# Performance work log

Hardware: AMD Instinct MI355X
Metric: run time of the kernel (lower is better)

The kernel has to match this reference:

```python
import jax, jax.numpy as jnp
import numpy as np
import math

B, S, D, H = 2, 2048, 1024, 16
DK = D // H


def setup_inputs() -> dict:
    key = jax.random.key(0)
    ks = jax.random.split(key, 11)
    f = jnp.float32
    return {
        "query": jax.random.normal(ks[0], (B, S, D), f),
        "key": jax.random.normal(ks[1], (B, S, D), f),
        "value": jax.random.normal(ks[2], (B, S, D), f),
        "wq": jax.random.normal(ks[3], (D, D), f) * 0.02,
        "bq": jnp.zeros((D,), f),
        "wk": jax.random.normal(ks[4], (D, D), f) * 0.02,
        "bk": jnp.zeros((D,), f),
        "wv": jax.random.normal(ks[5], (D, D), f) * 0.02,
        "bv": jnp.zeros((D,), f),
        "wo": jax.random.normal(ks[6], (D, D), f) * 0.02,
        "bo": jnp.zeros((D,), f),
    }


def reference(query, key, value, wq, bq, wk, bk, wv, bv, wo, bo):
    # Linear projections (torch Linear: y = x @ W.T + b)
    q = query @ wq.T + bq
    k = key @ wk.T + bk
    v = value @ wv.T + bv
    # [B,S,D] -> [B,H,S,DK]
    q = q.reshape(B, S, H, DK).transpose(0, 2, 1, 3)
    k = k.reshape(B, S, H, DK).transpose(0, 2, 1, 3)
    v = v.reshape(B, S, H, DK).transpose(0, 2, 1, 3)
    scores = jnp.einsum("bhqd,bhkd->bhqk", q, k) / math.sqrt(DK)
    causal = jnp.triu(jnp.ones((S, S), dtype=bool), k=1)  # strict upper triangle masked
    scores = jnp.where(causal, -jnp.inf, scores)
    attn = jax.nn.softmax(scores, axis=-1)  # dropout is identity in eval (p=0)
    x = jnp.einsum("bhqk,bhkd->bhqd", attn, v)
    x = x.transpose(0, 2, 1, 3).reshape(B, S, D)
    return x @ wo.T + bo
```

## Files before the change

kernel.cpp:

```cpp
#include <hip/hip_runtime.h>
#include <math.h>

#define BB 2
#define SS 2048
#define DD 1024
#define HH 16
#define DKK 64
#define MM (BB * SS)
#define KK DD
#define VSTR 2176

typedef __attribute__((ext_vector_type(8))) short short8;
typedef __attribute__((ext_vector_type(4))) float floatx4;

__device__ inline unsigned short f2bf(float x) {
    unsigned int u = __float_as_uint(x);
    u += 0x7fffu + ((u >> 16) & 1u);
    return (unsigned short)(u >> 16);
}

__device__ inline void cast4f(const float* __restrict__ in, unsigned short* __restrict__ out, int i) {
    const float4 v = *(const float4*)(in + i);
    unsigned long long pk = (unsigned long long)f2bf(v.x)
                          | ((unsigned long long)f2bf(v.y) << 16)
                          | ((unsigned long long)f2bf(v.z) << 32)
                          | ((unsigned long long)f2bf(v.w) << 48);
    *(unsigned long long*)(out + i) = pk;
}

__global__ __launch_bounds__(256) void cast3(const float* __restrict__ a, const float* __restrict__ b,
                                             const float* __restrict__ c,
                                             unsigned short* __restrict__ oa, unsigned short* __restrict__ ob,
                                             unsigned short* __restrict__ oc) {
    const int w = blockIdx.y;
    const float* in = (w == 0) ? a : (w == 1) ? b : c;
    unsigned short* out = (w == 0) ? oa : (w == 1) ? ob : oc;
    cast4f(in, out, (blockIdx.x * 256 + threadIdx.x) * 4);
}

__global__ __launch_bounds__(256) void cast4w(const float* __restrict__ a, const float* __restrict__ b,
                                              const float* __restrict__ c, const float* __restrict__ d,
                                              unsigned short* __restrict__ oa, unsigned short* __restrict__ ob,
                                              unsigned short* __restrict__ oc, unsigned short* __restrict__ od) {
    const int w = blockIdx.y;
    const float* in = (w == 0) ? a : (w == 1) ? b : (w == 2) ? c : d;
    unsigned short* out = (w == 0) ? oa : (w == 1) ? ob : (w == 2) ? oc : od;
    cast4f(in, out, (blockIdx.x * 256 + threadIdx.x) * 4);
}

#define GLDS(gp, lp) __builtin_amdgcn_global_load_lds( \
    (const __attribute__((address_space(1))) void*)(gp), \
    (__attribute__((address_space(3))) void*)(lp), 16, 0, 0)

__device__ __forceinline__ void gemm_body(const unsigned short* __restrict__ A,
                                          const unsigned short* __restrict__ W,
                                          const float* __restrict__ bias,
                                          void* __restrict__ Cout, int mode, int blk,
                                          unsigned short* As, unsigned short* Bs) {
    const int t    = threadIdx.x;
    const int lane = t & 63;
    const int wave = t >> 6;
    const int col  = lane & 15;
    const int quad = lane >> 4;

    const int m0  = (blk & 63) * 64;
    const int n0  = (blk >> 6) * 128;
    const int wm0 = (wave & 1) * 32;
    const int wn0 = (wave >> 1) * 64;

    const int sw = ((t & 3) ^ ((t >> 3) & 3)) * 8;
    const size_t arow = (size_t)(m0 + (t >> 2)) * KK + sw;
    const size_t brow = (size_t)(n0 + (t >> 2)) * KK + sw;
    const int rseg = (quad ^ ((col >> 1) & 3)) * 8;

    floatx4 acc[2][4] = {};

    GLDS(A + arow,           &As[(t >> 2) * 32 + sw]);
    GLDS(W + brow,           &Bs[(t >> 2) * 32 + sw]);
    GLDS(W + brow + 64 * KK, &Bs[(64 + (t >> 2)) * 32 + sw]);

    int cur = 0;
    for (int kb = 0; kb < KK / 32; ++kb) {
        __syncthreads();

        if (kb + 1 < KK / 32) {
            const int k0 = (kb + 1) * 32;
            const int nx = cur ^ 1;
            GLDS(A + arow + k0,           &As[nx * 64 * 32 + (t >> 2) * 32 + sw]);
            GLDS(W + brow + k0,           &Bs[nx * 128 * 32 + (t >> 2) * 32 + sw]);
            GLDS(W + brow + k0 + 64 * KK, &Bs[nx * 128 * 32 + (64 + (t >> 2)) * 32 + sw]);
        }

        const unsigned short* Ab = &As[cur * 64 * 32];
        const unsigned short* Bb = &Bs[cur * 128 * 32];
        short8 a[2], b[4];
        #pragma unroll
        for (int i = 0; i < 2; ++i)
            a[i] = *(const short8*)(Ab + (wm0 + i * 16 + col) * 32 + rseg);
        #pragma unroll
        for (int j = 0; j < 4; ++j)
            b[j] = *(const short8*)(Bb + (wn0 + j * 16 + col) * 32 + rseg);

        #pragma unroll
        for (int i = 0; i < 2; ++i)
            #pragma unroll
            for (int j = 0; j < 4; ++j)
                acc[i][j] = __builtin_amdgcn_mfma_f32_16x16x32_bf16(a[i], b[j], acc[i][j], 0, 0, 0);

        cur ^= 1;
    }

    #pragma unroll
    for (int i = 0; i < 2; ++i) {
        #pragma unroll
        for (int j = 0; j < 4; ++j) {
            const int n  = n0 + wn0 + j * 16 + col;
            const float bv = bias[n];
            const int h = n / DKK, dk = n % DKK;
            #pragma unroll
            for (int r = 0; r < 4; ++r) {
                const int m = m0 + wm0 + i * 16 + quad * 4 + r;
                const int bdx = m / SS, s = m % SS;
                const float v = acc[i][j][r] + bv;
                if (mode == 0) {
                    ((unsigned short*)Cout)[(((size_t)(bdx * HH + h)) * SS + s) * DKK + dk] = f2bf(v);
                } else if (mode == 1) {
                    ((unsigned short*)Cout)[(((size_t)(bdx * HH + h)) * DKK + dk) * VSTR + s] = f2bf(v);
                } else {
                    ((float*)Cout)[(size_t)m * DD + n] = v;
                }
            }
        }
    }
}

__global__ __launch_bounds__(256) void gemm_qkv(const unsigned short* __restrict__ qB,
                                                const unsigned short* __restrict__ kB,
                                                const unsigned short* __restrict__ vB,
                                                const unsigned short* __restrict__ wqB,
                                                const unsigned short* __restrict__ wkB,
                                                const unsigned short* __restrict__ wvB,
                                                const float* __restrict__ bq,
                                                const float* __restrict__ bk,
                                                const float* __restrict__ bv,
                                                unsigned short* __restrict__ Qh,
                                                unsigned short* __restrict__ Kh,
                                                unsigned short* __restrict__ Vt) {
    __shared__ __align__(16) unsigned short As[2 * 64 * 32];
    __shared__ __align__(16) unsigned short Bs[2 * 128 * 32];
    const int which = blockIdx.x >> 9;
    const int blk   = blockIdx.x & 511;
    if (which == 0)      gemm_body(qB, wqB, bq, Qh, 0, blk, As, Bs);
    else if (which == 1) gemm_body(kB, wkB, bk, Kh, 0, blk, As, Bs);
    else                 gemm_body(vB, wvB, bv, Vt, 1, blk, As, Bs);
}

__global__ __launch_bounds__(256) void gemm_out(const unsigned short* __restrict__ A,
                                                const unsigned short* __restrict__ W,
                                                const float* __restrict__ bias,
                                                float* __restrict__ C) {
    __shared__ __align__(16) unsigned short As[2 * 64 * 32];
    __shared__ __align__(16) unsigned short Bs[2 * 128 * 32];
    gemm_body(A, W, bias, C, 2, blockIdx.x, As, Bs);
}

#define C1 0.18033688011112042f
#define C2 11.541560327111707f

#define MFMA __builtin_amdgcn_mfma_f32_16x16x32_bf16

#define SOFTPV(j0v, vv)                                                                              \
    {                                                                                                \
        if ((j0v) + 31 > q0) {                                                                       \
            _Pragma("unroll")                                                                        \
            for (int r = 0; r < 4; ++r) {                                                            \
                const int row = q0 + quad * 4 + r;                                                   \
                const float p0 = ((j0v) + col      <= row) ? __builtin_exp2f(fmaf(sc0[r], C1, -C2)) : 0.f; \
                const float p1 = ((j0v) + 16 + col <= row) ? __builtin_exp2f(fmaf(sc1[r], C1, -C2)) : 0.f; \
                lp[r] += p0 + p1;                                                                    \
                Pw[(quad * 4 + r) * 40 + col]      = (unsigned short)(__float_as_uint(p0) >> 16);    \
                Pw[(quad * 4 + r) * 40 + col + 16] = (unsigned short)(__float_as_uint(p1) >> 16);    \
            }                                                                                        \
        } else {                                                                                     \
            _Pragma("unroll")                                                                        \
            for (int r = 0; r < 4; ++r) {                                                            \
                const float p0 = __builtin_exp2f(fmaf(sc0[r], C1, -C2));                             \
                const float p1 = __builtin_exp2f(fmaf(sc1[r], C1, -C2));                             \
                lp[r] += p0 + p1;                                                                    \
                Pw[(quad * 4 + r) * 40 + col]      = (unsigned short)(__float_as_uint(p0) >> 16);    \
                Pw[(quad * 4 + r) * 40 + col + 16] = (unsigned short)(__float_as_uint(p1) >> 16);    \
            }                                                                                        \
        }                                                                                            \
        const short8 pa = *(const short8*)(Pw + col * 40 + quad * 8);                                \
        o0 = MFMA(pa, vv##0, o0, 0, 0, 0);                                                           \
        o1 = MFMA(pa, vv##1, o1, 0, 0, 0);                                                           \
        o2 = MFMA(pa, vv##2, o2, 0, 0, 0);                                                           \
        o3 = MFMA(pa, vv##3, o3, 0, 0, 0);                                                           \
    }

__global__ __launch_bounds__(256) void attn_mfma(const unsigned short* __restrict__ Qh,
                                                 const unsigned short* __restrict__ Kh,
                                                 const unsigned short* __restrict__ Vt,
                                                 unsigned short* __restrict__ X) {
    __shared__ __align__(16) unsigned short Ks[2][32 * 64];
    __shared__ __align__(16) unsigned short Vs[2][64 * 32];
    __shared__ unsigned short Plds[4][16 * 40];

    const int t    = threadIdx.x;
    const int lane = t & 63;
    const int wave = t >> 6;
    const int col  = lane & 15;
    const int quad = lane >> 4;

    const int lin = blockIdx.x;
    const int bh  = (lin & 7) + 8 * ((lin >> 3) & 3);
    const int c   = 31 - (lin >> 5);
    const int b   = bh / HH, h = bh % HH;

    const unsigned short* Kb = Kh + (size_t)bh * SS * DKK;
    const unsigned short* Vb = Vt + (size_t)bh * DKK * VSTR;

    const int kRow = t >> 3;
    const int kSeg = ((t & 7) ^ (kRow & 7)) * 8;
    const int vRow = t >> 2;
    const int vSeg = (t & 3) * 8;

    const int q0 = c * 64 + wave * 16;
    unsigned short* Pw = &Plds[wave][0];

    const unsigned short* Qb = Qh + ((size_t)bh * SS + q0) * DKK;
    const short8 qa0 = *(const short8*)(Qb + (size_t)col * DKK + quad * 8);
    const short8 qa1 = *(const short8*)(Qb + (size_t)col * DKK + 32 + quad * 8);

    floatx4 o0 = {0.f, 0.f, 0.f, 0.f}, o1 = o0, o2 = o0, o3 = o0;
    float lp[4] = {0.f, 0.f, 0.f, 0.f};

    const int nkb = 2 * (c + 1);

    const int ks0 = ((quad     ^ (col & 7)) << 3);
    const int ks1 = (((quad|4) ^ (col & 7)) << 3);

    GLDS(Kb + (size_t)kRow * DKK + kSeg, &Ks[0][t * 8]);
    GLDS(Vb + (size_t)vRow * VSTR + vSeg, &Vs[0][t * 8]);

    int cur = 0;
    for (int kb = 0; kb < nkb; ++kb) {
        __syncthreads();

        if (kb + 1 < nkb) {
            const int jn = (kb + 1) * 32;
            const int nx = cur ^ 1;
            GLDS(Kb + (size_t)(jn + kRow) * DKK + kSeg, &Ks[nx][t * 8]);
            GLDS(Vb + (size_t)vRow * VSTR + jn + vSeg, &Vs[nx][t * 8]);
        }

        const int j0 = kb * 32;
        if (j0 < q0 + 16) {
            const unsigned short* Kp = &Ks[cur][0];
            const short8 k0 = *(const short8*)(Kp + col * 64 + ks0);
            const short8 k1 = *(const short8*)(Kp + col * 64 + ks1);
            const short8 k2 = *(const short8*)(Kp + (col + 16) * 64 + ks0);
            const short8 k3 = *(const short8*)(Kp + (col + 16) * 64 + ks1);

            floatx4 sc0 = {0.f, 0.f, 0.f, 0.f}, sc1 = sc0;
            sc0 = MFMA(qa0, k0, sc0, 0, 0, 0);
            sc0 = MFMA(qa1, k1, sc0, 0, 0, 0);
            sc1 = MFMA(qa0, k2, sc1, 0, 0, 0);
            sc1 = MFMA(qa1, k3, sc1, 0, 0, 0);

            const unsigned short* Vp = &Vs[cur][0];
            short8 vv0 = *(const short8*)(Vp + (col)      * 32 + quad * 8);
            short8 vv1 = *(const short8*)(Vp + (col + 16) * 32 + quad * 8);
            short8 vv2 = *(const short8*)(Vp + (col + 32) * 32 + quad * 8);
            short8 vv3 = *(const short8*)(Vp + (col + 48) * 32 + quad * 8);

            SOFTPV(j0, vv)
        }

        cur ^= 1;
    }

    #pragma unroll
    for (int r = 0; r < 4; ++r) {
        float s = lp[r];
        s += __shfl_xor(s, 1, 64);
        s += __shfl_xor(s, 2, 64);
        s += __shfl_xor(s, 4, 64);
        s += __shfl_xor(s, 8, 64);
        lp[r] = 1.f / s;
    }

    unsigned short* Xp = X + ((size_t)(b * SS + q0 + quad * 4)) * DD + h * DKK + col;
    #pragma unroll
    for (int r = 0; r < 4; ++r) {
        Xp[(size_t)r * DD + 0]  = f2bf(o0[r] * lp[r]);
        Xp[(size_t)r * DD + 16] = f2bf(o1[r] * lp[r]);
        Xp[(size_t)r * DD + 32] = f2bf(o2[r] * lp[r]);
        Xp[(size_t)r * DD + 48] = f2bf(o3[r] * lp[r]);
    }
}

extern "C" void kernel_launch(void* const* d_in, const int* in_sizes, int n_in,
                              void* d_out, int out_size, void* d_ws, size_t ws_size,
                              hipStream_t stream) {
    const float* query = (const float*)d_in[0];
    const float* key   = (const float*)d_in[1];
    const float* value = (const float*)d_in[2];
    const float* wq    = (const float*)d_in[3];
    const float* bq    = (const float*)d_in[4];
    const float* wk    = (const float*)d_in[5];
    const float* bk    = (const float*)d_in[6];
    const float* wv    = (const float*)d_in[7];
    const float* bv    = (const float*)d_in[8];
    const float* wo    = (const float*)d_in[9];
    const float* bo    = (const float*)d_in[10];

    char* ws = (char*)d_ws;
    const size_t MB = 1024 * 1024;
    unsigned short* qB  = (unsigned short*)(ws);
    unsigned short* kB  = (unsigned short*)(ws + 8 * MB);
    unsigned short* vB  = (unsigned short*)(ws + 16 * MB);
    unsigned short* wqB = (unsigned short*)(ws + 24 * MB);
    unsigned short* wkB = (unsigned short*)(ws + 26 * MB);
    unsigned short* wvB = (unsigned short*)(ws + 28 * MB);
    unsigned short* woB = (unsigned short*)(ws + 30 * MB);
    unsigned short* Qh  = (unsigned short*)(ws + 32 * MB);
    unsigned short* Kh  = (unsigned short*)(ws + 40 * MB);
    unsigned short* Vt  = (unsigned short*)(ws + 48 * MB);
    unsigned short* Xb  = qB;

    cast3<<<dim3(4096, 3), 256, 0, stream>>>(query, key, value, qB, kB, vB);
    cast4w<<<dim3(1024, 4), 256, 0, stream>>>(wq, wk, wv, wo, wqB, wkB, wvB, woB);

    gemm_qkv<<<1536, 256, 0, stream>>>(qB, kB, vB, wqB, wkB, wvB, bq, bk, bv, Qh, Kh, Vt);

    attn_mfma<<<1024, 256, 0, stream>>>(Qh, Kh, Vt, Xb);

    gemm_out<<<512, 256, 0, stream>>>(Xb, woB, bo, (float*)d_out);
}
```

Baseline: 250.3 us.

## Merge cast kernels, enlarge QKV GEMM tiles, restructure attention with 64-key stages

The two cast kernels become one launch. The QKV projection GEMM now uses its own kernel with 128x128 tiles (4x4 MFMA per wave) in place of the shared 64x128 body, halving the block count. Attention now stages 64 keys per iteration and computes the transposed product (K·Q, V·P), so each lane owns a query row: the row sum needs fewer shuffles, P goes to LDS as packed words, and outputs are written as vectorized uint2. The trade-off is more LDS and registers, which can lower occupancy.

```diff
diff --git a/kernel.cpp b/kernel.cpp
--- a/kernel.cpp
+++ b/kernel.cpp
@@ -19,6 +19,10 @@
     return (unsigned short)(u >> 16);
 }
 
+__device__ inline unsigned int pkbf(float a, float b) {
+    return (__float_as_uint(b) & 0xffff0000u) | (__float_as_uint(a) >> 16);
+}
+
 __device__ inline void cast4f(const float* __restrict__ in, unsigned short* __restrict__ out, int i) {
     const float4 v = *(const float4*)(in + i);
     unsigned long long pk = (unsigned long long)f2bf(v.x)
@@ -28,24 +32,30 @@
     *(unsigned long long*)(out + i) = pk;
 }
 
-__global__ __launch_bounds__(256) void cast3(const float* __restrict__ a, const float* __restrict__ b,
-                                             const float* __restrict__ c,
-                                             unsigned short* __restrict__ oa, unsigned short* __restrict__ ob,
-                                             unsigned short* __restrict__ oc) {
-    const int w = blockIdx.y;
-    const float* in = (w == 0) ? a : (w == 1) ? b : c;
-    unsigned short* out = (w == 0) ? oa : (w == 1) ? ob : oc;
-    cast4f(in, out, (blockIdx.x * 256 + threadIdx.x) * 4);
-}
-
-__global__ __launch_bounds__(256) void cast4w(const float* __restrict__ a, const float* __restrict__ b,
-                                              const float* __restrict__ c, const float* __restrict__ d,
-                                              unsigned short* __restrict__ oa, unsigned short* __restrict__ ob,
-                                              unsigned short* __restrict__ oc, unsigned short* __restrict__ od) {
-    const int w = blockIdx.y;
-    const float* in = (w == 0) ? a : (w == 1) ? b : (w == 2) ? c : d;
-    unsigned short* out = (w == 0) ? oa : (w == 1) ? ob : (w == 2) ? oc : od;
-    cast4f(in, out, (blockIdx.x * 256 + threadIdx.x) * 4);
+__global__ __launch_bounds__(256) void cast_all(const float* __restrict__ q, const float* __restrict__ k,
+                                                const float* __restrict__ v,
+                                                const float* __restrict__ wq, const float* __restrict__ wk,
+                                                const float* __restrict__ wv, const float* __restrict__ wo,
+                                                unsigned short* __restrict__ oq, unsigned short* __restrict__ ok,
+                                                unsigned short* __restrict__ ov,
+                                                unsigned short* __restrict__ owq, unsigned short* __restrict__ owk,
+                                                unsigned short* __restrict__ owv, unsigned short* __restrict__ owo) {
+    const int blk = blockIdx.x;
+    const float* in;
+    unsigned short* out;
+    int idx;
+    if (blk < 12288) {
+        const int w = blk >> 12;
+        idx = blk & 4095;
+        in  = (w == 0) ? q : (w == 1) ? k : v;
+        out = (w == 0) ? oq : (w == 1) ? ok : ov;
+    } else {
+        const int w = (blk - 12288) >> 10;
+        idx = (blk - 12288) & 1023;
+        in  = (w == 0) ? wq : (w == 1) ? wk : (w == 2) ? wv : wo;
+        out = (w == 0) ? owq : (w == 1) ? owk : (w == 2) ? owv : owo;
+    }
+    cast4f(in, out, (idx * 256 + threadIdx.x) * 4);
 }
 
 #define GLDS(gp, lp) __builtin_amdgcn_global_load_lds( \
@@ -116,22 +126,15 @@
         for (int j = 0; j < 4; ++j) {
             const int n  = n0 + wn0 + j * 16 + col;
             const float bv = bias[n];
-            const int h = n / DKK, dk = n % DKK;
             #pragma unroll
             for (int r = 0; r < 4; ++r) {
                 const int m = m0 + wm0 + i * 16 + quad * 4 + r;
-                const int bdx = m / SS, s = m % SS;
                 const float v = acc[i][j][r] + bv;
-                if (mode == 0) {
-                    ((unsigned short*)Cout)[(((size_t)(bdx * HH + h)) * SS + s) * DKK + dk] = f2bf(v);
-                } else if (mode == 1) {
-                    ((unsigned short*)Cout)[(((size_t)(bdx * HH + h)) * DKK + dk) * VSTR + s] = f2bf(v);
-                } else {
-                    ((float*)Cout)[(size_t)m * DD + n] = v;
-                }
+                ((float*)Cout)[(size_t)m * DD + n] = v;
             }
         }
     }
+    (void)mode;
 }
 
 __global__ __launch_bounds__(256) void gemm_qkv(const unsigned short* __restrict__ qB,
@@ -146,13 +149,91 @@
                                                 unsigned short* __restrict__ Qh,
                                                 unsigned short* __restrict__ Kh,
                                                 unsigned short* __restrict__ Vt) {
-    __shared__ __align__(16) unsigned short As[2 * 64 * 32];
+    __shared__ __align__(16) unsigned short As[2 * 128 * 32];
     __shared__ __align__(16) unsigned short Bs[2 * 128 * 32];
-    const int which = blockIdx.x >> 9;
-    const int blk   = blockIdx.x & 511;
-    if (which == 0)      gemm_body(qB, wqB, bq, Qh, 0, blk, As, Bs);
-    else if (which == 1) gemm_body(kB, wkB, bk, Kh, 0, blk, As, Bs);
-    else                 gemm_body(vB, wvB, bv, Vt, 1, blk, As, Bs);
+
+    const int which = blockIdx.x >> 8;
+    const int blk   = blockIdx.x & 255;
+    const unsigned short* A = (which == 0) ? qB : (which == 1) ? kB : vB;
+    const unsigned short* W = (which == 0) ? wqB : (which == 1) ? wkB : wvB;
+    const float* bias       = (which == 0) ? bq : (which == 1) ? bk : bv;
+
+    const int t    = threadIdx.x;
+    const int lane = t & 63;
+    const int wave = t >> 6;
+    const int col  = lane & 15;
+    const int quad = lane >> 4;
+
+    const int m0  = (blk & 31) * 128;
+    const int n0  = (blk >> 5) * 128;
+    const int wm0 = (wave & 1) * 64;
+    const int wn0 = (wave >> 1) * 64;
+
+    const int sw = ((t & 3) ^ ((t >> 3) & 3)) * 8;
+    const size_t arow = (size_t)(m0 + (t >> 2)) * KK + sw;
+    const size_t brow = (size_t)(n0 + (t >> 2)) * KK + sw;
+    const int rseg = (quad ^ ((col >> 1) & 3)) * 8;
+
+    floatx4 acc[4][4] = {};
+
+    GLDS(A + arow,           &As[(t >> 2) * 32 + sw]);
+    GLDS(A + arow + 64 * KK, &As[(64 + (t >> 2)) * 32 + sw]);
+    GLDS(W + brow,           &Bs[(t >> 2) * 32 + sw]);
+    GLDS(W + brow + 64 * KK, &Bs[(64 + (t >> 2)) * 32 + sw]);
+
+    int cur = 0;
+    for (int kb = 0; kb < KK / 32; ++kb) {
+        __syncthreads();
+
+        if (kb + 1 < KK / 32) {
+            const int k0 = (kb + 1) * 32;
+            const int nx = cur ^ 1;
+            GLDS(A + arow + k0,           &As[nx * 128 * 32 + (t >> 2) * 32 + sw]);
+            GLDS(A + arow + k0 + 64 * KK, &As[nx * 128 * 32 + (64 + (t >> 2)) * 32 + sw]);
+            GLDS(W + brow + k0,           &Bs[nx * 128 * 32 + (t >> 2) * 32 + sw]);
+            GLDS(W + brow + k0 + 64 * KK, &Bs[nx * 128 * 32 + (64 + (t >> 2)) * 32 + sw]);
+        }
+
+        const unsigned short* Ab = &As[cur * 128 * 32];
+        const unsigned short* Bb = &Bs[cur * 128 * 32];
+        short8 a[4], b[4];
+        #pragma unroll
+        for (int i = 0; i < 4; ++i)
+            a[i] = *(const short8*)(Ab + (wm0 + i * 16 + col) * 32 + rseg);
+        #pragma unroll
+        for (int j = 0; j < 4; ++j)
+            b[j] = *(const short8*)(Bb + (wn0 + j * 16 + col) * 32 + rseg);
+
+        #pragma unroll
+        for (int i = 0; i < 4; ++i)
+            #pragma unroll
+            for (int j = 0; j < 4; ++j)
+                acc[i][j] = __builtin_amdgcn_mfma_f32_16x16x32_bf16(a[i], b[j], acc[i][j], 0, 0, 0);
+
+        cur ^= 1;
+    }
+
+    #pragma unroll
+    for (int i = 0; i < 4; ++i) {
+        #pragma unroll
+        for (int j = 0; j < 4; ++j) {
+            const int n  = n0 + wn0 + j * 16 + col;
+            const float bv = bias[n];
+            const int h = n / DKK, dk = n % DKK;
+            #pragma unroll
+            for (int r = 0; r < 4; ++r) {
+                const int m = m0 + wm0 + i * 16 + quad * 4 + r;
+                const int bdx = m / SS, s = m % SS;
+                const float v = acc[i][j][r] + bv;
+                if (which != 2) {
+                    unsigned short* O = (which == 0) ? Qh : Kh;
+                    O[(((size_t)(bdx * HH + h)) * SS + s) * DKK + dk] = f2bf(v);
+                } else {
+                    Vt[(((size_t)(bdx * HH + h)) * DKK + dk) * VSTR + s] = f2bf(v);
+                }
+            }
+        }
+    }
 }
 
 __global__ __launch_bounds__(256) void gemm_out(const unsigned short* __restrict__ A,
@@ -166,45 +247,15 @@
 
 #define C1 0.18033688011112042f
 #define C2 11.541560327111707f
-
 #define MFMA __builtin_amdgcn_mfma_f32_16x16x32_bf16
-
-#define SOFTPV(j0v, vv)                                                                              \
-    {                                                                                                \
-        if ((j0v) + 31 > q0) {                                                                       \
-            _Pragma("unroll")                                                                        \
-            for (int r = 0; r < 4; ++r) {                                                            \
-                const int row = q0 + quad * 4 + r;                                                   \
-                const float p0 = ((j0v) + col      <= row) ? __builtin_exp2f(fmaf(sc0[r], C1, -C2)) : 0.f; \
-                const float p1 = ((j0v) + 16 + col <= row) ? __builtin_exp2f(fmaf(sc1[r], C1, -C2)) : 0.f; \
-                lp[r] += p0 + p1;                                                                    \
-                Pw[(quad * 4 + r) * 40 + col]      = (unsigned short)(__float_as_uint(p0) >> 16);    \
-                Pw[(quad * 4 + r) * 40 + col + 16] = (unsigned short)(__float_as_uint(p1) >> 16);    \
-            }                                                                                        \
-        } else {                                                                                     \
-            _Pragma("unroll")                                                                        \
-            for (int r = 0; r < 4; ++r) {                                                            \
-                const float p0 = __builtin_exp2f(fmaf(sc0[r], C1, -C2));                             \
-                const float p1 = __builtin_exp2f(fmaf(sc1[r], C1, -C2));                             \
-                lp[r] += p0 + p1;                                                                    \
-                Pw[(quad * 4 + r) * 40 + col]      = (unsigned short)(__float_as_uint(p0) >> 16);    \
-                Pw[(quad * 4 + r) * 40 + col + 16] = (unsigned short)(__float_as_uint(p1) >> 16);    \
-            }                                                                                        \
-        }                                                                                            \
-        const short8 pa = *(const short8*)(Pw + col * 40 + quad * 8);                                \
-        o0 = MFMA(pa, vv##0, o0, 0, 0, 0);                                                           \
-        o1 = MFMA(pa, vv##1, o1, 0, 0, 0);                                                           \
-        o2 = MFMA(pa, vv##2, o2, 0, 0, 0);                                                           \
-        o3 = MFMA(pa, vv##3, o3, 0, 0, 0);                                                           \
-    }
 
 __global__ __launch_bounds__(256) void attn_mfma(const unsigned short* __restrict__ Qh,
                                                  const unsigned short* __restrict__ Kh,
                                                  const unsigned short* __restrict__ Vt,
                                                  unsigned short* __restrict__ X) {
-    __shared__ __align__(16) unsigned short Ks[2][32 * 64];
-    __shared__ __align__(16) unsigned short Vs[2][64 * 32];
-    __shared__ unsigned short Plds[4][16 * 40];
+    __shared__ __align__(16) unsigned short Ks[2][64 * 64];
+    __shared__ __align__(16) unsigned short Vs[2][64 * 64];
+    __shared__ __align__(16) unsigned short Plds[4][16 * 40];
 
     const int t    = threadIdx.x;
     const int lane = t & 63;
@@ -220,10 +271,10 @@
     const unsigned short* Kb = Kh + (size_t)bh * SS * DKK;
     const unsigned short* Vb = Vt + (size_t)bh * DKK * VSTR;
 
-    const int kRow = t >> 3;
-    const int kSeg = ((t & 7) ^ (kRow & 7)) * 8;
-    const int vRow = t >> 2;
-    const int vSeg = (t & 3) * 8;
+    const int r0  = t >> 3;
+    const int r1  = (t + 256) >> 3;
+    const int sg0 = ((t & 7) ^ (r0 & 7)) * 8;
+    const int sg1 = ((t & 7) ^ (r1 & 7)) * 8;
 
     const int q0 = c * 64 + wave * 16;
     unsigned short* Pw = &Plds[wave][0];
@@ -233,70 +284,106 @@
     const short8 qa1 = *(const short8*)(Qb + (size_t)col * DKK + 32 + quad * 8);
 
     floatx4 o0 = {0.f, 0.f, 0.f, 0.f}, o1 = o0, o2 = o0, o3 = o0;
-    float lp[4] = {0.f, 0.f, 0.f, 0.f};
-
-    const int nkb = 2 * (c + 1);
-
-    const int ks0 = ((quad     ^ (col & 7)) << 3);
-    const int ks1 = (((quad|4) ^ (col & 7)) << 3);
-
-    GLDS(Kb + (size_t)kRow * DKK + kSeg, &Ks[0][t * 8]);
-    GLDS(Vb + (size_t)vRow * VSTR + vSeg, &Vs[0][t * 8]);
+    float lp = 0.f;
+
+    const int nst = c + 1;
+
+    const int ksA = ((quad)      ^ (col & 7)) * 8;
+    const int ksB = ((quad | 4)  ^ (col & 7)) * 8;
+
+    GLDS(Kb + (size_t)r0 * DKK + sg0,  &Ks[0][t * 8]);
+    GLDS(Kb + (size_t)r1 * DKK + sg1,  &Ks[0][(t + 256) * 8]);
+    GLDS(Vb + (size_t)r0 * VSTR + sg0, &Vs[0][t * 8]);
+    GLDS(Vb + (size_t)r1 * VSTR + sg1, &Vs[0][(t + 256) * 8]);
 
     int cur = 0;
-    for (int kb = 0; kb < nkb; ++kb) {
+    for (int kb = 0; kb < nst; ++kb) {
         __syncthreads();
 
-        if (kb + 1 < nkb) {
-            const int jn = (kb + 1) * 32;
+        if (kb + 1 < nst) {
+            const int jn = (kb + 1) * 64;
             const int nx = cur ^ 1;
-            GLDS(Kb + (size_t)(jn + kRow) * DKK + kSeg, &Ks[nx][t * 8]);
-            GLDS(Vb + (size_t)vRow * VSTR + jn + vSeg, &Vs[nx][t * 8]);
-        }
-
-        const int j0 = kb * 32;
-        if (j0 < q0 + 16) {
-            const unsigned short* Kp = &Ks[cur][0];
-            const short8 k0 = *(const short8*)(Kp + col * 64 + ks0);
-            const short8 k1 = *(const short8*)(Kp + col * 64 + ks1);
-            const short8 k2 = *(const short8*)(Kp + (col + 16) * 64 + ks0);
-            const short8 k3 = *(const short8*)(Kp + (col + 16) * 64 + ks1);
-
-            floatx4 sc0 = {0.f, 0.f, 0.f, 0.f}, sc1 = sc0;
-            sc0 = MFMA(qa0, k0, sc0, 0, 0, 0);
-            sc0 = MFMA(qa1, k1, sc0, 0, 0, 0);
-            sc1 = MFMA(qa0, k2, sc1, 0, 0, 0);
-            sc1 = MFMA(qa1, k3, sc1, 0, 0, 0);
-
-            const unsigned short* Vp = &Vs[cur][0];
-            short8 vv0 = *(const short8*)(Vp + (col)      * 32 + quad * 8);
-            short8 vv1 = *(const short8*)(Vp + (col + 16) * 32 + quad * 8);
-            short8 vv2 = *(const short8*)(Vp + (col + 32) * 32 + quad * 8);
-            short8 vv3 = *(const short8*)(Vp + (col + 48) * 32 + quad * 8);
-
-            SOFTPV(j0, vv)
+            GLDS(Kb + (size_t)(jn + r0) * DKK + sg0,  &Ks[nx][t * 8]);
+            GLDS(Kb + (size_t)(jn + r1) * DKK + sg1,  &Ks[nx][(t + 256) * 8]);
+            GLDS(Vb + (size_t)r0 * VSTR + jn + sg0,   &Vs[nx][t * 8]);
+            GLDS(Vb + (size_t)r1 * VSTR + jn + sg1,   &Vs[nx][(t + 256) * 8]);
+        }
+
+        const unsigned short* Kp = &Ks[cur][0];
+        const unsigned short* Vp = &Vs[cur][0];
+
+        #pragma unroll
+        for (int hh = 0; hh < 2; ++hh) {
+            const int j0 = kb * 64 + hh * 32;
+            if (j0 < q0 + 16) {
+                const short8 k0 = *(const short8*)(Kp + (hh * 32 + col) * 64 + ksA);
+                const short8 k1 = *(const short8*)(Kp + (hh * 32 + col) * 64 + ksB);
+                const short8 k2 = *(const short8*)(Kp + (hh * 32 + col + 16) * 64 + ksA);
+                const short8 k3 = *(const short8*)(Kp + (hh * 32 + col + 16) * 64 + ksB);
+
+                floatx4 t0 = {0.f, 0.f, 0.f, 0.f}, t1 = t0;
+                t0 = MFMA(k0, qa0, t0, 0, 0, 0);
+                t0 = MFMA(k1, qa1, t0, 0, 0, 0);
+                t1 = MFMA(k2, qa0, t1, 0, 0, 0);
+                t1 = MFMA(k3, qa1, t1, 0, 0, 0);
+
+                float p[8];
+                if (j0 + 31 > q0) {
+                    const int lim = q0 + col - j0;
+                    #pragma unroll
+                    for (int r = 0; r < 4; ++r) {
+                        p[r]     = (quad * 4 + r      <= lim) ? __builtin_exp2f(fmaf(t0[r], C1, -C2)) : 0.f;
+                        p[4 + r] = (16 + quad * 4 + r <= lim) ? __builtin_exp2f(fmaf(t1[r], C1, -C2)) : 0.f;
+                    }
+                } else {
+                    #pragma unroll
+                    for (int r = 0; r < 4; ++r) {
+                        p[r]     = __builtin_exp2f(fmaf(t0[r], C1, -C2));
+                        p[4 + r] = __builtin_exp2f(fmaf(t1[r], C1, -C2));
+                    }
+                }
+                lp += (p[0] + p[1]) + (p[2] + p[3]) + (p[4] + p[5]) + (p[6] + p[7]);
+
+                uint2 w0 = { pkbf(p[0], p[1]), pkbf(p[2], p[3]) };
+                uint2 w1 = { pkbf(p[4], p[5]), pkbf(p[6], p[7]) };
+                *(uint2*)(Pw + col * 40 + quad * 4)      = w0;
+                *(uint2*)(Pw + col * 40 + 16 + quad * 4) = w1;
+
+                const short8 pb = *(const short8*)(Pw + col * 40 + quad * 8);
+                const int vs = hh ? ksB : ksA;
+                const short8 v0 = *(const short8*)(Vp + (col)      * 64 + vs);
+                const short8 v1 = *(const short8*)(Vp + (col + 16) * 64 + vs);
+                const short8 v2 = *(const short8*)(Vp + (col + 32) * 64 + vs);
+                const short8 v3 = *(const short8*)(Vp + (col + 48) * 64 + vs);
+                o0 = MFMA(v0, pb, o0, 0, 0, 0);
+                o1 = MFMA(v1, pb, o1, 0, 0, 0);
+                o2 = MFMA(v2, pb, o2, 0, 0, 0);
+                o3 = MFMA(v3, pb, o3, 0, 0, 0);
+            }
         }
 
         cur ^= 1;
     }
 
-    #pragma unroll
-    for (int r = 0; r < 4; ++r) {
-        float s = lp[r];
-        s += __shfl_xor(s, 1, 64);
-        s += __shfl_xor(s, 2, 64);
-        s += __shfl_xor(s, 4, 64);
-        s += __shfl_xor(s, 8, 64);
-        lp[r] = 1.f / s;
-    }
-
-    unsigned short* Xp = X + ((size_t)(b * SS + q0 + quad * 4)) * DD + h * DKK + col;
-    #pragma unroll
-    for (int r = 0; r < 4; ++r) {
-        Xp[(size_t)r * DD + 0]  = f2bf(o0[r] * lp[r]);
-        Xp[(size_t)r * DD + 16] = f2bf(o1[r] * lp[r]);
-        Xp[(size_t)r * DD + 32] = f2bf(o2[r] * lp[r]);
-        Xp[(size_t)r * DD + 48] = f2bf(o3[r] * lp[r]);
+    lp += __shfl_xor(lp, 16, 64);
+    lp += __shfl_xor(lp, 32, 64);
+    const float li = 1.f / lp;
+
+    unsigned short* Xp = X + ((size_t)(b * SS + q0 + col)) * DD + h * DKK + quad * 4;
+    {
+        uint2 w;
+        w.x = (unsigned int)f2bf(o0[0] * li) | ((unsigned int)f2bf(o0[1] * li) << 16);
+        w.y = (unsigned int)f2bf(o0[2] * li) | ((unsigned int)f2bf(o0[3] * li) << 16);
+        *(uint2*)(Xp + 0) = w;
+        w.x = (unsigned int)f2bf(o1[0] * li) | ((unsigned int)f2bf(o1[1] * li) << 16);
+        w.y = (unsigned int)f2bf(o1[2] * li) | ((unsigned int)f2bf(o1[3] * li) << 16);
+        *(uint2*)(Xp + 16) = w;
+        w.x = (unsigned int)f2bf(o2[0] * li) | ((unsigned int)f2bf(o2[1] * li) << 16);
+        w.y = (unsigned int)f2bf(o2[2] * li) | ((unsigned int)f2bf(o2[3] * li) << 16);
+        *(uint2*)(Xp + 32) = w;
+        w.x = (unsigned int)f2bf(o3[0] * li) | ((unsigned int)f2bf(o3[1] * li) << 16);
+        w.y = (unsigned int)f2bf(o3[2] * li) | ((unsigned int)f2bf(o3[3] * li) << 16);
+        *(uint2*)(Xp + 48) = w;
     }
 }
 
@@ -329,10 +416,10 @@
     unsigned short* Vt  = (unsigned short*)(ws + 48 * MB);
     unsigned short* Xb  = qB;
 
-    cast3<<<dim3(4096, 3), 256, 0, stream>>>(query, key, value, qB, kB, vB);
-    cast4w<<<dim3(1024, 4), 256, 0, stream>>>(wq, wk, wv, wo, wqB, wkB, wvB, woB);
-
-    gemm_qkv<<<1536, 256, 0, stream>>>(qB, kB, vB, wqB, wkB, wvB, bq, bk, bv, Qh, Kh, Vt);
+    cast_all<<<16384, 256, 0, stream>>>(query, key, value, wq, wk, wv, wo,
+                                        qB, kB, vB, wqB, wkB, wvB, woB);
+
+    gemm_qkv<<<768, 256, 0, stream>>>(qB, kB, vB, wqB, wkB, wvB, bq, bk, bv, Qh, Kh, Vt);
 
     attn_mfma<<<1024, 256, 0, stream>>>(Qh, Kh, Vt, Xb);
 
```

Result: faster. 227.2 us (-9.2%).
